# Kernel optimization log

Hardware: AMD Instinct MI355X
Metric: run time of the kernel (lower is better)

## Reference

```python
import jax, jax.numpy as jnp
import numpy as np

N = 2097152          # fine mesh elements
C = 64               # feature channels
M = 524288           # coarse segments (4:1 pooling)


def setup_inputs() -> dict:
    key = jax.random.key(0)
    k1, k2 = jax.random.split(key)
    mesh_ids = jax.random.randint(k1, (N,), 0, M, dtype=jnp.int32)
    sources = jax.random.normal(k2, (N, C), dtype=jnp.float32)
    return {"mesh_ids": mesh_ids, "sources": sources, "num_segments": M}


def reference(mesh_ids, sources, num_segments):
    # Segment-mean pooling: average all source rows sharing the same mesh id.
    sums = jax.ops.segment_sum(sources, mesh_ids, num_segments=num_segments)   # [M, C]
    counts = jax.ops.segment_sum(
        jnp.ones((sources.shape[0],), dtype=sources.dtype), mesh_ids,
        num_segments=num_segments)                                             # [M]
    # Empty segments get 0 output (avoid div-by-zero).
    return sums / jnp.maximum(counts, 1.0)[:, None]
```

## Files before the change

kernel.cpp:

```cpp
#include <hip/hip_runtime.h>


#define SLOTS   16
#define OVF_CAP 8192

typedef float f32x4 __attribute__((ext_vector_type(4)));
typedef int   i32x4 __attribute__((ext_vector_type(4)));

__global__ void scatter_slots(const int* __restrict__ ids,
                              int* __restrict__ counts,
                              int* __restrict__ slots,
                              int* __restrict__ ovf,
                              int n4) {
    const int i = blockIdx.x * blockDim.x + threadIdx.x;
    if (i >= n4) return;
    const i32x4 v = __builtin_nontemporal_load(reinterpret_cast<const i32x4*>(ids) + i);
    const int r0 = i << 2;
    #pragma unroll
    for (int j = 0; j < 4; ++j) {
        const int id = v[j];
        const int k  = atomicAdd(&counts[id], 1);
        if (k < SLOTS) {
            slots[id * SLOTS + k] = r0 + j;
        } else {
            int p = atomicAdd(ovf, 1);
            if (p < OVF_CAP) { ovf[1 + 2 * p] = r0 + j; ovf[2 + 2 * p] = id; }
        }
    }
}

__global__ void gather_mean(const float* __restrict__ src,
                            const int* __restrict__ slots,
                            const int* __restrict__ counts,
                            float* __restrict__ out, int m) {
    const int t = blockIdx.x * blockDim.x + threadIdx.x;
    const int p = t >> 4;
    const int q = t & 15;
    const int sA = 2 * p, sB = 2 * p + 1;
    if (sB >= m) return;
    const int2 c2 = *reinterpret_cast<const int2*>(counts + sA);
    const int cA = c2.x, cB = c2.y;
    const int lA = cA < SLOTS ? cA : SLOTS;
    const int lB = cB < SLOTS ? cB : SLOTS;
    const long bA = (long)sA * SLOTS, bB = (long)sB * SLOTS;
    const f32x4* s4 = reinterpret_cast<const f32x4*>(src);
    f32x4 aA = (f32x4)(0.f), aB = (f32x4)(0.f);
    const int lmax = lA > lB ? lA : lB;
    for (int kk = 0; kk < lmax; kk += 4) {
        const i32x4 xA = *reinterpret_cast<const i32x4*>(slots + bA + kk);
        const i32x4 xB = *reinterpret_cast<const i32x4*>(slots + bB + kk);
        const int rA = lA - kk, rB = lB - kk;
        f32x4 vA0 = (f32x4)(0.f), vA1 = vA0, vA2 = vA0, vA3 = vA0;
        f32x4 vB0 = vA0, vB1 = vA0, vB2 = vA0, vB3 = vA0;
        if (rA > 0) vA0 = __builtin_nontemporal_load(s4 + ((long)xA[0] * 16 + q));
        if (rB > 0) vB0 = __builtin_nontemporal_load(s4 + ((long)xB[0] * 16 + q));
        if (rA > 1) vA1 = __builtin_nontemporal_load(s4 + ((long)xA[1] * 16 + q));
        if (rB > 1) vB1 = __builtin_nontemporal_load(s4 + ((long)xB[1] * 16 + q));
        if (rA > 2) vA2 = __builtin_nontemporal_load(s4 + ((long)xA[2] * 16 + q));
        if (rB > 2) vB2 = __builtin_nontemporal_load(s4 + ((long)xB[2] * 16 + q));
        if (rA > 3) vA3 = __builtin_nontemporal_load(s4 + ((long)xA[3] * 16 + q));
        if (rB > 3) vB3 = __builtin_nontemporal_load(s4 + ((long)xB[3] * 16 + q));
        aA += (vA0 + vA1) + (vA2 + vA3);
        aB += (vB0 + vB1) + (vB2 + vB3);
    }
    aA *= 1.0f / (float)(cA > 1 ? cA : 1);
    aB *= 1.0f / (float)(cB > 1 ? cB : 1);
    __builtin_nontemporal_store(aA, reinterpret_cast<f32x4*>(out) + ((long)sA * 16 + q));
    __builtin_nontemporal_store(aB, reinterpret_cast<f32x4*>(out) + ((long)sB * 16 + q));
}

__global__ void ovf_fix(const float* __restrict__ src,
                        const int* __restrict__ counts,
                        const int* __restrict__ ovf,
                        float* __restrict__ out) {
    int novf = ovf[0];
    if (novf > OVF_CAP) novf = OVF_CAP;
    const int total  = novf * 16;
    const int stride = gridDim.x * blockDim.x;
    for (int t = blockIdx.x * blockDim.x + threadIdx.x; t < total; t += stride) {
        const int e = t >> 4, q = t & 15;
        const int row = ovf[1 + 2 * e], id = ovf[2 + 2 * e];
        const float rcp = 1.0f / (float)counts[id];
        const float4 v = reinterpret_cast<const float4*>(src)[(long)row * 16 + q];
        float* o = out + (long)id * 64 + q * 4;
        unsafeAtomicAdd(o + 0, v.x * rcp);
        unsafeAtomicAdd(o + 1, v.y * rcp);
        unsafeAtomicAdd(o + 2, v.z * rcp);
        unsafeAtomicAdd(o + 3, v.w * rcp);
    }
}

extern "C" void kernel_launch(void* const* d_in, const int* in_sizes, int n_in,
                              void* d_out, int out_size, void* d_ws, size_t ws_size,
                              hipStream_t stream) {
    const int*   ids = (const int*)d_in[0];
    const float* src = (const float*)d_in[1];
    float*       out = (float*)d_out;

    const int n = in_sizes[0];
    const int m = out_size / 64;

    int* counts = (int*)d_ws;
    int* ovf    = counts + m;
    int* slots  = ovf + (1 + 2 * OVF_CAP);

    (void)hipMemsetAsync(counts, 0, (size_t)m * sizeof(int), stream);
    (void)hipMemsetAsync(ovf, 0, sizeof(int), stream);

    const int n4 = n >> 2;
    scatter_slots<<<(n4 + 255) / 256, 256, 0, stream>>>(ids, counts, slots, ovf, n4);
    const int pairs = m / 2;
    gather_mean<<<(pairs * 16 + 255) / 256, 256, 0, stream>>>(src, slots, counts, out, m);
    ovf_fix<<<64, 256, 0, stream>>>(src, counts, ovf, out);
}
```

Before: 314.9 us.

## Fuse memset, scatter, gather and overflow fix into one cooperative persistent kernel

```diff
diff --git a/kernel.cpp b/kernel.cpp
--- a/kernel.cpp
+++ b/kernel.cpp
@@ -1,4 +1,5 @@
 #include <hip/hip_runtime.h>
+#include <hip/hip_cooperative_groups.h>
 
 
 #define SLOTS   16
@@ -7,109 +8,128 @@
 typedef float f32x4 __attribute__((ext_vector_type(4)));
 typedef int   i32x4 __attribute__((ext_vector_type(4)));
 
-__global__ void scatter_slots(const int* __restrict__ ids,
-                              int* __restrict__ counts,
-                              int* __restrict__ slots,
-                              int* __restrict__ ovf,
-                              int n4) {
-    const int i = blockIdx.x * blockDim.x + threadIdx.x;
-    if (i >= n4) return;
-    const i32x4 v = __builtin_nontemporal_load(reinterpret_cast<const i32x4*>(ids) + i);
-    const int r0 = i << 2;
-    #pragma unroll
-    for (int j = 0; j < 4; ++j) {
-        const int id = v[j];
-        const int k  = atomicAdd(&counts[id], 1);
-        if (k < SLOTS) {
-            slots[id * SLOTS + k] = r0 + j;
-        } else {
-            int p = atomicAdd(ovf, 1);
-            if (p < OVF_CAP) { ovf[1 + 2 * p] = r0 + j; ovf[2 + 2 * p] = id; }
+namespace cg = cooperative_groups;
+
+__global__ void __launch_bounds__(256, 2) fused_pool(
+    const int* __restrict__ ids, const float* __restrict__ src,
+    int* __restrict__ counts, int* __restrict__ slots, int* __restrict__ ovf,
+    float* __restrict__ out, int n, int m)
+{
+    cg::grid_group grid = cg::this_grid();
+    const int tid = blockIdx.x * blockDim.x + threadIdx.x;
+    const int nthreads = gridDim.x * blockDim.x;
+
+    {
+        i32x4* c4 = reinterpret_cast<i32x4*>(counts);
+        const int m4 = m >> 2;
+        for (int i = tid; i < m4; i += nthreads) c4[i] = (i32x4)(0);
+        if (tid == 0) ovf[0] = 0;
+    }
+    grid.sync();
+
+    {
+        const int n4 = n >> 2;
+        for (int i = tid; i < n4; i += nthreads) {
+            const i32x4 v = __builtin_nontemporal_load(
+                reinterpret_cast<const i32x4*>(ids) + i);
+            const int r0 = i << 2;
+            #pragma unroll
+            for (int j = 0; j < 4; ++j) {
+                const int id = v[j];
+                const int k  = atomicAdd(&counts[id], 1);
+                if (k < SLOTS) {
+                    slots[id * SLOTS + k] = r0 + j;
+                } else {
+                    int p = atomicAdd(ovf, 1);
+                    if (p < OVF_CAP) { ovf[1 + 2 * p] = r0 + j; ovf[2 + 2 * p] = id; }
+                }
+            }
         }
     }
-}
+    grid.sync();
 
-__global__ void gather_mean(const float* __restrict__ src,
-                            const int* __restrict__ slots,
-                            const int* __restrict__ counts,
-                            float* __restrict__ out, int m) {
-    const int t = blockIdx.x * blockDim.x + threadIdx.x;
-    const int p = t >> 4;
-    const int q = t & 15;
-    const int sA = 2 * p, sB = 2 * p + 1;
-    if (sB >= m) return;
-    const int2 c2 = *reinterpret_cast<const int2*>(counts + sA);
-    const int cA = c2.x, cB = c2.y;
-    const int lA = cA < SLOTS ? cA : SLOTS;
-    const int lB = cB < SLOTS ? cB : SLOTS;
-    const long bA = (long)sA * SLOTS, bB = (long)sB * SLOTS;
-    const f32x4* s4 = reinterpret_cast<const f32x4*>(src);
-    f32x4 aA = (f32x4)(0.f), aB = (f32x4)(0.f);
-    const int lmax = lA > lB ? lA : lB;
-    for (int kk = 0; kk < lmax; kk += 4) {
-        const i32x4 xA = *reinterpret_cast<const i32x4*>(slots + bA + kk);
-        const i32x4 xB = *reinterpret_cast<const i32x4*>(slots + bB + kk);
-        const int rA = lA - kk, rB = lB - kk;
-        f32x4 vA0 = (f32x4)(0.f), vA1 = vA0, vA2 = vA0, vA3 = vA0;
-        f32x4 vB0 = vA0, vB1 = vA0, vB2 = vA0, vB3 = vA0;
-        if (rA > 0) vA0 = __builtin_nontemporal_load(s4 + ((long)xA[0] * 16 + q));
-        if (rB > 0) vB0 = __builtin_nontemporal_load(s4 + ((long)xB[0] * 16 + q));
-        if (rA > 1) vA1 = __builtin_nontemporal_load(s4 + ((long)xA[1] * 16 + q));
-        if (rB > 1) vB1 = __builtin_nontemporal_load(s4 + ((long)xB[1] * 16 + q));
-        if (rA > 2) vA2 = __builtin_nontemporal_load(s4 + ((long)xA[2] * 16 + q));
-        if (rB > 2) vB2 = __builtin_nontemporal_load(s4 + ((long)xB[2] * 16 + q));
-        if (rA > 3) vA3 = __builtin_nontemporal_load(s4 + ((long)xA[3] * 16 + q));
-        if (rB > 3) vB3 = __builtin_nontemporal_load(s4 + ((long)xB[3] * 16 + q));
-        aA += (vA0 + vA1) + (vA2 + vA3);
-        aB += (vB0 + vB1) + (vB2 + vB3);
+    {
+        const int  pairs = m >> 1;
+        const long tasks = (long)pairs * 16;
+        const f32x4* s4 = reinterpret_cast<const f32x4*>(src);
+        for (long t = tid; t < tasks; t += nthreads) {
+            const int p = (int)(t >> 4);
+            const int q = (int)(t & 15);
+            const int sA = 2 * p, sB = 2 * p + 1;
+            const int2 c2 = *reinterpret_cast<const int2*>(counts + sA);
+            const int cA = c2.x, cB = c2.y;
+            const int lA = cA < SLOTS ? cA : SLOTS;
+            const int lB = cB < SLOTS ? cB : SLOTS;
+            const long bA = (long)sA * SLOTS, bB = (long)sB * SLOTS;
+            f32x4 aA = (f32x4)(0.f), aB = (f32x4)(0.f);
+            const int lmax = lA > lB ? lA : lB;
+            for (int kk = 0; kk < lmax; kk += 4) {
+                const i32x4 xA = *reinterpret_cast<const i32x4*>(slots + bA + kk);
+                const i32x4 xB = *reinterpret_cast<const i32x4*>(slots + bB + kk);
+                const int rA = lA - kk, rB = lB - kk;
+                f32x4 vA0 = (f32x4)(0.f), vA1 = vA0, vA2 = vA0, vA3 = vA0;
+                f32x4 vB0 = vA0, vB1 = vA0, vB2 = vA0, vB3 = vA0;
+                if (rA > 0) vA0 = __builtin_nontemporal_load(s4 + ((long)xA[0] * 16 + q));
+                if (rB > 0) vB0 = __builtin_nontemporal_load(s4 + ((long)xB[0] * 16 + q));
+                if (rA > 1) vA1 = __builtin_nontemporal_load(s4 + ((long)xA[1] * 16 + q));
+                if (rB > 1) vB1 = __builtin_nontemporal_load(s4 + ((long)xB[1] * 16 + q));
+                if (rA > 2) vA2 = __builtin_nontemporal_load(s4 + ((long)xA[2] * 16 + q));
+                if (rB > 2) vB2 = __builtin_nontemporal_load(s4 + ((long)xB[2] * 16 + q));
+                if (rA > 3) vA3 = __builtin_nontemporal_load(s4 + ((long)xA[3] * 16 + q));
+                if (rB > 3) vB3 = __builtin_nontemporal_load(s4 + ((long)xB[3] * 16 + q));
+                aA += (vA0 + vA1) + (vA2 + vA3);
+                aB += (vB0 + vB1) + (vB2 + vB3);
+            }
+            aA *= 1.0f / (float)(cA > 1 ? cA : 1);
+            aB *= 1.0f / (float)(cB > 1 ? cB : 1);
+            __builtin_nontemporal_store(aA, reinterpret_cast<f32x4*>(out) + ((long)sA * 16 + q));
+            __builtin_nontemporal_store(aB, reinterpret_cast<f32x4*>(out) + ((long)sB * 16 + q));
+        }
     }
-    aA *= 1.0f / (float)(cA > 1 ? cA : 1);
-    aB *= 1.0f / (float)(cB > 1 ? cB : 1);
-    __builtin_nontemporal_store(aA, reinterpret_cast<f32x4*>(out) + ((long)sA * 16 + q));
-    __builtin_nontemporal_store(aB, reinterpret_cast<f32x4*>(out) + ((long)sB * 16 + q));
-}
+    grid.sync();
 
-__global__ void ovf_fix(const float* __restrict__ src,
-                        const int* __restrict__ counts,
-                        const int* __restrict__ ovf,
-                        float* __restrict__ out) {
-    int novf = ovf[0];
-    if (novf > OVF_CAP) novf = OVF_CAP;
-    const int total  = novf * 16;
-    const int stride = gridDim.x * blockDim.x;
-    for (int t = blockIdx.x * blockDim.x + threadIdx.x; t < total; t += stride) {
-        const int e = t >> 4, q = t & 15;
-        const int row = ovf[1 + 2 * e], id = ovf[2 + 2 * e];
-        const float rcp = 1.0f / (float)counts[id];
-        const float4 v = reinterpret_cast<const float4*>(src)[(long)row * 16 + q];
-        float* o = out + (long)id * 64 + q * 4;
-        unsafeAtomicAdd(o + 0, v.x * rcp);
-        unsafeAtomicAdd(o + 1, v.y * rcp);
-        unsafeAtomicAdd(o + 2, v.z * rcp);
-        unsafeAtomicAdd(o + 3, v.w * rcp);
+    {
+        int novf = ovf[0];
+        if (novf > OVF_CAP) novf = OVF_CAP;
+        const int total = novf * 16;
+        for (int t = tid; t < total; t += nthreads) {
+            const int e = t >> 4, q = t & 15;
+            const int row = ovf[1 + 2 * e], id = ovf[2 + 2 * e];
+            const float rcp = 1.0f / (float)counts[id];
+            const float4 v = reinterpret_cast<const float4*>(src)[(long)row * 16 + q];
+            float* o = out + (long)id * 64 + q * 4;
+            unsafeAtomicAdd(o + 0, v.x * rcp);
+            unsafeAtomicAdd(o + 1, v.y * rcp);
+            unsafeAtomicAdd(o + 2, v.z * rcp);
+            unsafeAtomicAdd(o + 3, v.w * rcp);
+        }
     }
 }
 
 extern "C" void kernel_launch(void* const* d_in, const int* in_sizes, int n_in,
                               void* d_out, int out_size, void* d_ws, size_t ws_size,
                               hipStream_t stream) {
-    const int*   ids = (const int*)d_in[0];
-    const float* src = (const float*)d_in[1];
-    float*       out = (float*)d_out;
+    const int* ids_c = (const int*)d_in[0];
+    const float* src_c = (const float*)d_in[1];
+    float* out = (float*)d_out;
 
-    const int n = in_sizes[0];
-    const int m = out_size / 64;
+    int n = in_sizes[0];
+    int m = out_size / 64;
 
     int* counts = (int*)d_ws;
     int* ovf    = counts + m;
     int* slots  = ovf + (1 + 2 * OVF_CAP);
 
-    (void)hipMemsetAsync(counts, 0, (size_t)m * sizeof(int), stream);
-    (void)hipMemsetAsync(ovf, 0, sizeof(int), stream);
+    int blocksPerCU = 0;
+    (void)hipOccupancyMaxActiveBlocksPerMultiprocessor(
+        &blocksPerCU, (const void*)fused_pool, 256, 0);
+    if (blocksPerCU < 1) blocksPerCU = 1;
+    int gridBlocks = blocksPerCU * 256;
+    if (gridBlocks > 2048) gridBlocks = 2048;
 
-    const int n4 = n >> 2;
-    scatter_slots<<<(n4 + 255) / 256, 256, 0, stream>>>(ids, counts, slots, ovf, n4);
-    const int pairs = m / 2;
-    gather_mean<<<(pairs * 16 + 255) / 256, 256, 0, stream>>>(src, slots, counts, out, m);
-    ovf_fix<<<64, 256, 0, stream>>>(src, counts, ovf, out);
+    const int* ids = ids_c; const float* src = src_c;
+    void* args[] = {(void*)&ids, (void*)&src, (void*)&counts, (void*)&slots,
+                    (void*)&ovf, (void*)&out, (void*)&n, (void*)&m};
+    (void)hipLaunchCooperativeKernel((void*)fused_pool, dim3(gridBlocks), dim3(256),
+                                     args, 0, stream);
 }
```

After: 629.2 us. +99.8%, slower.

## Issue first eight gathers unconditionally and fold overflow handling into gather kernel

Applied to the files above, without the earlier changes.

```diff
diff --git a/kernel.cpp b/kernel.cpp
--- a/kernel.cpp
+++ b/kernel.cpp
@@ -6,6 +6,14 @@
 
 typedef float f32x4 __attribute__((ext_vector_type(4)));
 typedef int   i32x4 __attribute__((ext_vector_type(4)));
+
+__global__ void zero_counts(int* __restrict__ counts, int* __restrict__ ovf, int m4) {
+    const int stride = gridDim.x * blockDim.x;
+    i32x4* c4 = reinterpret_cast<i32x4*>(counts);
+    for (int i = blockIdx.x * blockDim.x + threadIdx.x; i < m4; i += stride)
+        c4[i] = (i32x4)(0);
+    if (blockIdx.x == 0 && threadIdx.x == 0) ovf[0] = 0;
+}
 
 __global__ void scatter_slots(const int* __restrict__ ids,
                               int* __restrict__ counts,
@@ -32,62 +40,72 @@
 __global__ void gather_mean(const float* __restrict__ src,
                             const int* __restrict__ slots,
                             const int* __restrict__ counts,
+                            const int* __restrict__ ovf,
                             float* __restrict__ out, int m) {
     const int t = blockIdx.x * blockDim.x + threadIdx.x;
     const int p = t >> 4;
     const int q = t & 15;
     const int sA = 2 * p, sB = 2 * p + 1;
     if (sB >= m) return;
-    const int2 c2 = *reinterpret_cast<const int2*>(counts + sA);
+    const long bA = (long)sA * SLOTS, bB = (long)sB * SLOTS;
+    const i32x4 xA0 = *reinterpret_cast<const i32x4*>(slots + bA);
+    const i32x4 xB0 = *reinterpret_cast<const i32x4*>(slots + bB);
+    const i32x4 xA1 = *reinterpret_cast<const i32x4*>(slots + bA + 4);
+    const i32x4 xB1 = *reinterpret_cast<const i32x4*>(slots + bB + 4);
+    const int2  c2  = *reinterpret_cast<const int2*>(counts + sA);
     const int cA = c2.x, cB = c2.y;
     const int lA = cA < SLOTS ? cA : SLOTS;
     const int lB = cB < SLOTS ? cB : SLOTS;
-    const long bA = (long)sA * SLOTS, bB = (long)sB * SLOTS;
     const f32x4* s4 = reinterpret_cast<const f32x4*>(src);
+
+    int rA[8], rB[8];
+    #pragma unroll
+    for (int j = 0; j < 4; ++j) {
+        rA[j]     = (lA > j)     ? xA0[j] : 0;
+        rA[j + 4] = (lA > j + 4) ? xA1[j] : 0;
+        rB[j]     = (lB > j)     ? xB0[j] : 0;
+        rB[j + 4] = (lB > j + 4) ? xB1[j] : 0;
+    }
+    f32x4 vA[8], vB[8];
+    #pragma unroll
+    for (int j = 0; j < 8; ++j) {
+        vA[j] = s4[(long)rA[j] * 16 + q];
+        vB[j] = s4[(long)rB[j] * 16 + q];
+    }
     f32x4 aA = (f32x4)(0.f), aB = (f32x4)(0.f);
-    const int lmax = lA > lB ? lA : lB;
-    for (int kk = 0; kk < lmax; kk += 4) {
-        const i32x4 xA = *reinterpret_cast<const i32x4*>(slots + bA + kk);
-        const i32x4 xB = *reinterpret_cast<const i32x4*>(slots + bB + kk);
-        const int rA = lA - kk, rB = lB - kk;
-        f32x4 vA0 = (f32x4)(0.f), vA1 = vA0, vA2 = vA0, vA3 = vA0;
-        f32x4 vB0 = vA0, vB1 = vA0, vB2 = vA0, vB3 = vA0;
-        if (rA > 0) vA0 = __builtin_nontemporal_load(s4 + ((long)xA[0] * 16 + q));
-        if (rB > 0) vB0 = __builtin_nontemporal_load(s4 + ((long)xB[0] * 16 + q));
-        if (rA > 1) vA1 = __builtin_nontemporal_load(s4 + ((long)xA[1] * 16 + q));
-        if (rB > 1) vB1 = __builtin_nontemporal_load(s4 + ((long)xB[1] * 16 + q));
-        if (rA > 2) vA2 = __builtin_nontemporal_load(s4 + ((long)xA[2] * 16 + q));
-        if (rB > 2) vB2 = __builtin_nontemporal_load(s4 + ((long)xB[2] * 16 + q));
-        if (rA > 3) vA3 = __builtin_nontemporal_load(s4 + ((long)xA[3] * 16 + q));
-        if (rB > 3) vB3 = __builtin_nontemporal_load(s4 + ((long)xB[3] * 16 + q));
-        aA += (vA0 + vA1) + (vA2 + vA3);
-        aB += (vB0 + vB1) + (vB2 + vB3);
+    #pragma unroll
+    for (int j = 0; j < 8; ++j) {
+        aA += vA[j] * ((lA > j) ? 1.0f : 0.0f);
+        aB += vB[j] * ((lB > j) ? 1.0f : 0.0f);
+    }
+
+    if ((lA > 8) | (lB > 8)) {
+        const int lmax = lA > lB ? lA : lB;
+        for (int kk = 8; kk < lmax; kk += 4) {
+            const i32x4 yA = *reinterpret_cast<const i32x4*>(slots + bA + kk);
+            const i32x4 yB = *reinterpret_cast<const i32x4*>(slots + bB + kk);
+            #pragma unroll
+            for (int j = 0; j < 4; ++j) {
+                const int wA = (lA > kk + j) ? yA[j] : 0;
+                const int wB = (lB > kk + j) ? yB[j] : 0;
+                aA += s4[(long)wA * 16 + q] * ((lA > kk + j) ? 1.0f : 0.0f);
+                aB += s4[(long)wB * 16 + q] * ((lB > kk + j) ? 1.0f : 0.0f);
+            }
+        }
+    }
+    if ((cA > SLOTS) | (cB > SLOTS)) {
+        int novf = ovf[0];
+        if (novf > OVF_CAP) novf = OVF_CAP;
+        for (int e = 0; e < novf; ++e) {
+            const int row = ovf[1 + 2 * e], id = ovf[2 + 2 * e];
+            if (id == sA) aA += s4[(long)row * 16 + q];
+            if (id == sB) aB += s4[(long)row * 16 + q];
+        }
     }
     aA *= 1.0f / (float)(cA > 1 ? cA : 1);
     aB *= 1.0f / (float)(cB > 1 ? cB : 1);
     __builtin_nontemporal_store(aA, reinterpret_cast<f32x4*>(out) + ((long)sA * 16 + q));
     __builtin_nontemporal_store(aB, reinterpret_cast<f32x4*>(out) + ((long)sB * 16 + q));
-}
-
-__global__ void ovf_fix(const float* __restrict__ src,
-                        const int* __restrict__ counts,
-                        const int* __restrict__ ovf,
-                        float* __restrict__ out) {
-    int novf = ovf[0];
-    if (novf > OVF_CAP) novf = OVF_CAP;
-    const int total  = novf * 16;
-    const int stride = gridDim.x * blockDim.x;
-    for (int t = blockIdx.x * blockDim.x + threadIdx.x; t < total; t += stride) {
-        const int e = t >> 4, q = t & 15;
-        const int row = ovf[1 + 2 * e], id = ovf[2 + 2 * e];
-        const float rcp = 1.0f / (float)counts[id];
-        const float4 v = reinterpret_cast<const float4*>(src)[(long)row * 16 + q];
-        float* o = out + (long)id * 64 + q * 4;
-        unsafeAtomicAdd(o + 0, v.x * rcp);
-        unsafeAtomicAdd(o + 1, v.y * rcp);
-        unsafeAtomicAdd(o + 2, v.z * rcp);
-        unsafeAtomicAdd(o + 3, v.w * rcp);
-    }
 }
 
 extern "C" void kernel_launch(void* const* d_in, const int* in_sizes, int n_in,
@@ -104,12 +122,9 @@
     int* ovf    = counts + m;
     int* slots  = ovf + (1 + 2 * OVF_CAP);
 
-    (void)hipMemsetAsync(counts, 0, (size_t)m * sizeof(int), stream);
-    (void)hipMemsetAsync(ovf, 0, sizeof(int), stream);
-
+    zero_counts<<<256, 256, 0, stream>>>(counts, ovf, m >> 2);
     const int n4 = n >> 2;
     scatter_slots<<<(n4 + 255) / 256, 256, 0, stream>>>(ids, counts, slots, ovf, n4);
     const int pairs = m / 2;
-    gather_mean<<<(pairs * 16 + 255) / 256, 256, 0, stream>>>(src, slots, counts, out, m);
-    ovf_fix<<<64, 256, 0, stream>>>(src, counts, ovf, out);
+    gather_mean<<<(pairs * 16 + 255) / 256, 256, 0, stream>>>(src, slots, counts, ovf, out, m);
 }
```

Result: faster. 308.7 us (-2.0%).
